# Kernel tuning notes

Measured on AMD Instinct MI355X. Metric: run time of the kernel, lower is better.

Reference implementation:

```python
import jax, jax.numpy as jnp
import numpy as np

# Dims: T timesteps, B batch, C channels, HID expert hidden, E experts, K top-k
T, B, C, HID, E, K, H, W = 4, 8, 256, 1024, 8, 2, 14, 14
EPS = 1e-5       # BatchNorm eps
ALPHA = 4.0      # spikingjelly sigmoid surrogate alpha
V_TH = 1.0       # LIF threshold (spikingjelly default), v_reset = 0.0


@jax.custom_vjp
def spike_fn(u):
    # Heaviside forward, sigmoid-surrogate backward (spikingjelly surrogate.Sigmoid)
    return (u >= 0.0).astype(u.dtype)

def _spike_fwd(u):
    return (u >= 0.0).astype(u.dtype), u

def _spike_bwd(u, g):
    s = jax.nn.sigmoid(ALPHA * u)
    return (g * ALPHA * s * (1.0 - s),)

spike_fn.defvjp(_spike_fwd, _spike_bwd)


def lif(x, tau):
    """MultiStepLIFNode with hard reset (v_reset=0), detach_reset=True.
    x: (T, B, C, H, W) -> spikes of same shape."""
    def step(v, xt):
        h = v + (xt - v) / tau                      # charge
        s = spike_fn(h - V_TH)                      # fire
        v_new = h * (1.0 - jax.lax.stop_gradient(s))  # hard reset, detached spike
        return v_new, s
    _, spikes = jax.lax.scan(step, jnp.zeros_like(x[0]), x)
    return spikes


def conv1x1(x, w, b):
    # x: (T,B,Cin,H,W), w: (Cout,Cin), b: (Cout,) -- 1x1 conv == channel GEMM
    return jnp.einsum('tbchw,oc->tbohw', x, w) + b[None, None, :, None, None]


def bn(x, g, b, m, v, axis):
    # inference-mode BatchNorm with running stats, per-channel on `axis`
    shp = [1] * x.ndim
    shp[axis] = -1
    scale = g.reshape(shp) / jnp.sqrt(v.reshape(shp) + EPS)
    return (x - m.reshape(shp)) * scale + b.reshape(shp)


def expert(x, tau, w1, b1, g1, be1, m1, v1, w2, b2, g2, be2, m2, v2):
    # MS_MLP_Expert.forward: lif -> conv1x1 -> bn -> lif -> conv1x1 -> bn (no residual)
    s1 = lif(x, tau)
    h = bn(conv1x1(s1, w1, b1), g1, be1, m1, v1, axis=2)  # (T,B,HID,H,W)
    s2 = lif(h, tau)
    return bn(conv1x1(s2, w2, b2), g2, be2, m2, v2, axis=2)  # (T,B,C,H,W)


def setup_inputs() -> dict:
    key = jax.random.key(0)
    ks = jax.random.split(key, 16)
    d = {}
    d['x'] = jax.random.normal(ks[0], (T, B, C, H, W), jnp.float32)
    # router (Conv2d(C, E, 1) + BatchNorm2d(E))
    d['router_w'] = jax.random.normal(ks[1], (E, C), jnp.float32) / np.sqrt(C)
    d['router_b'] = jax.random.normal(ks[2], (E,), jnp.float32) * 0.01
    d['rbn_g'] = 1.0 + 0.1 * jax.random.normal(ks[3], (E,), jnp.float32)
    d['rbn_b'] = 0.1 * jax.random.normal(ks[4], (E,), jnp.float32)
    d['rbn_m'] = 0.1 * jax.random.normal(ks[5], (E,), jnp.float32)
    d['rbn_v'] = jax.random.uniform(ks[6], (E,), jnp.float32, 0.5, 1.5)
    # stacked expert params (leading expert axis E)
    d['fc1_w'] = jax.random.normal(ks[7], (E, HID, C), jnp.float32) / np.sqrt(C)
    d['fc1_b'] = 0.01 * jax.random.normal(ks[8], (E, HID), jnp.float32)
    d['bn1_g'] = 1.0 + 0.1 * jax.random.normal(ks[9], (E, HID), jnp.float32)
    d['bn1_b'] = 0.1 * jax.random.normal(ks[10], (E, HID), jnp.float32)
    d['bn1_m'] = 0.1 * jax.random.normal(ks[11], (E, HID), jnp.float32)
    d['bn1_v'] = jax.random.uniform(ks[12], (E, HID), jnp.float32, 0.5, 1.5)
    d['fc2_w'] = jax.random.normal(ks[13], (E, C, HID), jnp.float32) / np.sqrt(HID)
    d['fc2_b'] = 0.01 * jax.random.normal(ks[14], (E, C), jnp.float32)
    d['bn2_g'] = 1.0 + 0.1 * jax.random.normal(ks[15], (E, C), jnp.float32)
    k2 = jax.random.split(jax.random.fold_in(key, 1), 3)
    d['bn2_b'] = 0.1 * jax.random.normal(k2[0], (E, C), jnp.float32)
    d['bn2_m'] = 0.1 * jax.random.normal(k2[1], (E, C), jnp.float32)
    d['bn2_v'] = jax.random.uniform(k2[2], (E, C), jnp.float32, 0.5, 1.5)
    # expert taus: linspace(tau_min=1.5, tau_max=4.0, num_experts)
    d['taus'] = jnp.linspace(1.5, 4.0, E, dtype=jnp.float32)
    return d


def reference(x, router_w, router_b, rbn_g, rbn_b, rbn_m, rbn_v,
              fc1_w, fc1_b, bn1_g, bn1_b, bn1_m, bn1_v,
              fc2_w, fc2_b, bn2_g, bn2_b, bn2_m, bn2_v, taus):
    b_sz = x.shape[1]
    # ---- TemporalRouter ----
    xm = x.mean(axis=0)                                           # (B,C,H,W)
    r = jnp.einsum('bchw,ec->behw', xm, router_w) + router_b[None, :, None, None]
    r = bn(r, rbn_g, rbn_b, rbn_m, rbn_v, axis=1)
    logits = r.mean(axis=(-2, -1))                                # (B,E)
    probs = jax.nn.softmax(logits, axis=-1)
    topw, topi = jax.lax.top_k(probs, K)                          # (B,K)
    topw = topw / topw.sum(axis=-1, keepdims=True)
    # dense combine weights (B,E): top-k entries, 0 elsewhere; detached as in torch
    Wd = jnp.zeros((b_sz, E), x.dtype).at[jnp.arange(b_sz)[:, None], topi].add(topw)
    Wd = jax.lax.stop_gradient(Wd)
    # ---- Experts (dense dispatch: each expert over full batch, masked combine) ----
    outs = jax.vmap(expert, in_axes=(None,) + (0,) * 13)(
        x, taus, fc1_w, fc1_b, bn1_g, bn1_b, bn1_m, bn1_v,
        fc2_w, fc2_b, bn2_g, bn2_b, bn2_m, bn2_v)                 # (E,T,B,C,H,W)
    moe = jnp.einsum('etbchw,be->tbchw', outs, Wd)
    return x + moe
```

## Files before the change

kernel.cpp:

```cpp
#include <hip/hip_runtime.h>
#include <hip/hip_bf16.h>
#include <math.h>

#define T_ 4
#define B_ 8
#define C_ 256
#define HID_ 1024
#define E_ 8
#define K_ 2
#define HW_ 196
#define M_ 784
#define NPAIR_ 16
#define EPS_ 1e-5f

typedef __attribute__((ext_vector_type(8))) short bf16x8;
typedef __attribute__((ext_vector_type(8))) unsigned short u16x8;
typedef __attribute__((ext_vector_type(4))) float f32x4;

__device__ inline unsigned short f2bf(float f){
  union { float f; unsigned u; } v; v.f = f;
  unsigned u = v.u;
  unsigned r = u + 0x7FFFu + ((u >> 16) & 1u);
  return (unsigned short)(r >> 16);
}
__device__ inline float bf2f(unsigned short h){
  union { unsigned u; float f; } v; v.u = ((unsigned)h) << 16;
  return v.f;
}

__global__ __launch_bounds__(256) void wconv_kernel(const float* __restrict__ w,
    unsigned short* __restrict__ hi, unsigned short* __restrict__ lo, int n){
  int i = blockIdx.x * 256 + threadIdx.x;
  if (i >= n) return;
  float f = w[i];
  unsigned short h = f2bf(f);
  hi[i] = h;
  lo[i] = f2bf(f - bf2f(h));
}

__global__ __launch_bounds__(64) void xbar_kernel(const float* __restrict__ x,
                                                  float* __restrict__ xbar){
  int bc = blockIdx.x;
  int l = threadIdx.x;
  float s = 0.f;
  for (int t = 0; t < T_; t++){
    const float* p = x + ((size_t)(t * B_ * C_) + bc) * HW_;
    for (int i = l; i < HW_; i += 64) s += p[i];
  }
  for (int off = 32; off > 0; off >>= 1) s += __shfl_down(s, off, 64);
  if (l == 0) xbar[bc] = s * (1.0f / (T_ * HW_));
}

__global__ __launch_bounds__(64) void router_kernel(const float* __restrict__ xbar,
    const float* __restrict__ rw, const float* __restrict__ rb,
    const float* __restrict__ rg, const float* __restrict__ rbb,
    const float* __restrict__ rm, const float* __restrict__ rv,
    int* __restrict__ sel_e, float* __restrict__ sel_w){
  __shared__ float lg[64];
  const int tid = threadIdx.x;
  const int b = tid >> 3, e = tid & 7;
  float dot = 0.f;
  for (int c = 0; c < C_; c++) dot += xbar[b * C_ + c] * rw[e * C_ + c];
  dot += rb[e];
  float sc = rg[e] / sqrtf(rv[e] + EPS_);
  lg[tid] = (dot - rm[e]) * sc + rbb[e];
  __syncthreads();
  if (e == 0){
    float l[E_], mx = -1e30f;
    for (int i = 0; i < E_; i++){ l[i] = lg[b * 8 + i]; mx = fmaxf(mx, l[i]); }
    float p[E_];
    for (int i = 0; i < E_; i++) p[i] = expf(l[i] - mx);
    int i1 = 0;
    for (int i = 1; i < E_; i++) if (p[i] > p[i1]) i1 = i;
    int i2 = (i1 == 0) ? 1 : 0;
    for (int i = 0; i < E_; i++) if (i != i1 && p[i] > p[i2]) i2 = i;
    float denom = p[i1] + p[i2];
    sel_e[b * 2]     = i1; sel_w[b * 2]     = p[i1] / denom;
    sel_e[b * 2 + 1] = i2; sel_w[b * 2 + 1] = p[i2] / denom;
  }
}

__global__ __launch_bounds__(256) void lif1_kernel(const float* __restrict__ x,
    const int* __restrict__ sel_e, const float* __restrict__ taus,
    unsigned short* __restrict__ s1){
  const int hw = blockIdx.x;
  const int pair = blockIdx.y;
  const int c = threadIdx.x;
  const int b = pair >> 1;
  const float tau = taus[sel_e[pair]];
  float v = 0.f;
  #pragma unroll
  for (int t = 0; t < T_; t++){
    float xv = x[((size_t)(t * B_ + b) * C_ + c) * HW_ + hw];
    float h = v + (xv - v) / tau;
    float s = (h >= 1.0f) ? 1.0f : 0.0f;
    v = h * (1.0f - s);
    s1[((size_t)pair * M_ + hw * 4 + t) * C_ + c] =
        (s > 0.5f) ? (unsigned short)0x3F80 : (unsigned short)0;
  }
}

__global__ __launch_bounds__(256) void g1_kernel(
    const unsigned short* __restrict__ s1,
    const unsigned short* __restrict__ w1h, const unsigned short* __restrict__ w1l,
    const float* __restrict__ fc1_b,
    const float* __restrict__ bn1_g, const float* __restrict__ bn1_b,
    const float* __restrict__ bn1_m, const float* __restrict__ bn1_v,
    const int* __restrict__ sel_e, const float* __restrict__ taus,
    unsigned short* __restrict__ s2)
{
  __shared__ __align__(16) unsigned short lA[64 * 40];
  __shared__ __align__(16) unsigned short lBh[64 * 40];
  __shared__ __align__(16) unsigned short lBl[64 * 40];
  const int nt = blockIdx.x, mt = blockIdx.y, pair = blockIdx.z;
  const int e = sel_e[pair];
  const int m0 = mt * 64, n0 = nt * 64;
  const int tid = threadIdx.x;
  const int row = tid >> 2, seg = tid & 3;
  const int lane = tid & 63, wv = tid >> 6;
  const int koff = (lane >> 4) * 8;
  const unsigned short* s1p = s1 + (size_t)pair * (M_ * C_);
  const unsigned short* bhp = w1h + ((size_t)e * HID_ + n0 + row) * C_ + seg * 8;
  const unsigned short* blp = w1l + ((size_t)e * HID_ + n0 + row) * C_ + seg * 8;
  f32x4 acc[4] = {};
  for (int kk = 0; kk < C_; kk += 32){
    int r = m0 + row;
    u16x8 av = {};
    if (r < M_) av = *(const u16x8*)(s1p + (size_t)r * C_ + kk + seg * 8);
    *(u16x8*)(lA  + row * 40 + seg * 8) = av;
    *(u16x8*)(lBh + row * 40 + seg * 8) = *(const u16x8*)(bhp + kk);
    *(u16x8*)(lBl + row * 40 + seg * 8) = *(const u16x8*)(blp + kk);
    __syncthreads();
    bf16x8 a = *(const bf16x8*)(lA + (wv * 16 + (lane & 15)) * 40 + koff);
    #pragma unroll
    for (int cb = 0; cb < 4; cb++){
      bf16x8 bh = *(const bf16x8*)(lBh + (cb * 16 + (lane & 15)) * 40 + koff);
      bf16x8 bl = *(const bf16x8*)(lBl + (cb * 16 + (lane & 15)) * 40 + koff);
      acc[cb] = __builtin_amdgcn_mfma_f32_16x16x32_bf16(a, bh, acc[cb], 0, 0, 0);
      acc[cb] = __builtin_amdgcn_mfma_f32_16x16x32_bf16(a, bl, acc[cb], 0, 0, 0);
    }
    __syncthreads();
  }
  const float tau = taus[e];
  const int rbase = m0 + wv * 16 + ((lane >> 4) << 2);
  if (rbase < M_){
    #pragma unroll
    for (int cb = 0; cb < 4; cb++){
      int col = n0 + cb * 16 + (lane & 15);
      int pi = e * HID_ + col;
      float sc = bn1_g[pi] / sqrtf(bn1_v[pi] + EPS_);
      float mm = bn1_m[pi], bb = bn1_b[pi], cbias = fc1_b[pi];
      float v = 0.f;
      #pragma unroll
      for (int t = 0; t < 4; t++){
        float z = acc[cb][t] + cbias;
        float hin = (z - mm) * sc + bb;
        float h = v + (hin - v) / tau;
        float s = (h >= 1.0f) ? 1.0f : 0.0f;
        v = h * (1.0f - s);
        s2[((size_t)pair * M_ + rbase + t) * HID_ + col] =
            (s > 0.5f) ? (unsigned short)0x3F80 : (unsigned short)0;
      }
    }
  }
}

__global__ __launch_bounds__(256) void g2_kernel(
    const unsigned short* __restrict__ s2,
    const unsigned short* __restrict__ w2h, const unsigned short* __restrict__ w2l,
    const float* __restrict__ fc2_b,
    const float* __restrict__ bn2_g, const float* __restrict__ bn2_b,
    const float* __restrict__ bn2_m, const float* __restrict__ bn2_v,
    const int* __restrict__ sel_e, const float* __restrict__ sel_w,
    const float* __restrict__ x, float* __restrict__ out)
{
  __shared__ __align__(16) unsigned short lA[64 * 40];
  __shared__ __align__(16) unsigned short lBh[64 * 40];
  __shared__ __align__(16) unsigned short lBl[64 * 40];
  const int nt = blockIdx.x, mt = blockIdx.y, b = blockIdx.z;
  const int m0 = mt * 64, n0 = nt * 64;
  const int tid = threadIdx.x;
  const int row = tid >> 2, seg = tid & 3;
  const int lane = tid & 63, wv = tid >> 6;
  const int koff = (lane >> 4) * 8;
  f32x4 res[4] = {};
  for (int slot = 0; slot < 2; slot++){
    const int pair = b * 2 + slot;
    const int e = sel_e[pair];
    const float wgt = sel_w[pair];
    const unsigned short* s2p = s2 + (size_t)pair * (M_ * HID_);
    const unsigned short* bhp = w2h + ((size_t)e * C_ + n0 + row) * HID_ + seg * 8;
    const unsigned short* blp = w2l + ((size_t)e * C_ + n0 + row) * HID_ + seg * 8;
    f32x4 acc[4] = {};
    for (int kk = 0; kk < HID_; kk += 32){
      int r = m0 + row;
      u16x8 av = {};
      if (r < M_) av = *(const u16x8*)(s2p + (size_t)r * HID_ + kk + seg * 8);
      *(u16x8*)(lA  + row * 40 + seg * 8) = av;
      *(u16x8*)(lBh + row * 40 + seg * 8) = *(const u16x8*)(bhp + kk);
      *(u16x8*)(lBl + row * 40 + seg * 8) = *(const u16x8*)(blp + kk);
      __syncthreads();
      bf16x8 a = *(const bf16x8*)(lA + (wv * 16 + (lane & 15)) * 40 + koff);
      #pragma unroll
      for (int cb = 0; cb < 4; cb++){
        bf16x8 bh = *(const bf16x8*)(lBh + (cb * 16 + (lane & 15)) * 40 + koff);
        bf16x8 bl = *(const bf16x8*)(lBl + (cb * 16 + (lane & 15)) * 40 + koff);
        acc[cb] = __builtin_amdgcn_mfma_f32_16x16x32_bf16(a, bh, acc[cb], 0, 0, 0);
        acc[cb] = __builtin_amdgcn_mfma_f32_16x16x32_bf16(a, bl, acc[cb], 0, 0, 0);
      }
      __syncthreads();
    }
    #pragma unroll
    for (int cb = 0; cb < 4; cb++){
      int col = n0 + cb * 16 + (lane & 15);
      int pi = e * C_ + col;
      float sc = bn2_g[pi] / sqrtf(bn2_v[pi] + EPS_);
      float mm = bn2_m[pi], bb = bn2_b[pi], cbias = fc2_b[pi];
      #pragma unroll
      for (int t = 0; t < 4; t++){
        float z = acc[cb][t] + cbias;
        float y = (z - mm) * sc + bb;
        res[cb][t] += wgt * y;
      }
    }
  }
  const int rbase = m0 + wv * 16 + ((lane >> 4) << 2);
  if (rbase < M_){
    const int hw = rbase >> 2;
    #pragma unroll
    for (int cb = 0; cb < 4; cb++){
      int col = n0 + cb * 16 + (lane & 15);
      #pragma unroll
      for (int t = 0; t < 4; t++){
        size_t oi = ((size_t)(t * B_ + b) * C_ + col) * HW_ + hw;
        out[oi] = x[oi] + res[cb][t];
      }
    }
  }
}

extern "C" void kernel_launch(void* const* d_in, const int* in_sizes, int n_in,
                              void* d_out, int out_size, void* d_ws, size_t ws_size,
                              hipStream_t stream){
  const float* x     = (const float*)d_in[0];
  const float* rw    = (const float*)d_in[1];
  const float* rb    = (const float*)d_in[2];
  const float* rg    = (const float*)d_in[3];
  const float* rbb   = (const float*)d_in[4];
  const float* rm    = (const float*)d_in[5];
  const float* rv    = (const float*)d_in[6];
  const float* fc1_w = (const float*)d_in[7];
  const float* fc1_b = (const float*)d_in[8];
  const float* bn1_g = (const float*)d_in[9];
  const float* bn1_b = (const float*)d_in[10];
  const float* bn1_m = (const float*)d_in[11];
  const float* bn1_v = (const float*)d_in[12];
  const float* fc2_w = (const float*)d_in[13];
  const float* fc2_b = (const float*)d_in[14];
  const float* bn2_g = (const float*)d_in[15];
  const float* bn2_b = (const float*)d_in[16];
  const float* bn2_m = (const float*)d_in[17];
  const float* bn2_v = (const float*)d_in[18];
  const float* taus  = (const float*)d_in[19];
  float* out = (float*)d_out;

  char* ws = (char*)d_ws;
  size_t off = 0;
  auto alloc = [&](size_t bytes) -> char* {
    char* p = ws + off;
    off = (off + bytes + 255) & ~(size_t)255;
    return p;
  };
  const int NW = E_ * HID_ * C_;
  unsigned short* w1h = (unsigned short*)alloc((size_t)NW * 2);
  unsigned short* w1l = (unsigned short*)alloc((size_t)NW * 2);
  unsigned short* w2h = (unsigned short*)alloc((size_t)NW * 2);
  unsigned short* w2l = (unsigned short*)alloc((size_t)NW * 2);
  unsigned short* s1  = (unsigned short*)alloc((size_t)NPAIR_ * M_ * C_ * 2);
  unsigned short* s2  = (unsigned short*)alloc((size_t)NPAIR_ * M_ * HID_ * 2);
  float* xbar  = (float*)alloc(B_ * C_ * 4);
  int*   sel_e = (int*)alloc(NPAIR_ * 4);
  float* sel_w = (float*)alloc(NPAIR_ * 4);
  (void)ws_size; (void)in_sizes; (void)n_in; (void)out_size;

  wconv_kernel<<<(NW + 255) / 256, 256, 0, stream>>>(fc1_w, w1h, w1l, NW);
  wconv_kernel<<<(NW + 255) / 256, 256, 0, stream>>>(fc2_w, w2h, w2l, NW);
  xbar_kernel<<<B_ * C_, 64, 0, stream>>>(x, xbar);
  router_kernel<<<1, 64, 0, stream>>>(xbar, rw, rb, rg, rbb, rm, rv, sel_e, sel_w);
  lif1_kernel<<<dim3(HW_, NPAIR_), 256, 0, stream>>>(x, sel_e, taus, s1);
  g1_kernel<<<dim3(HID_ / 64, (M_ + 63) / 64, NPAIR_), 256, 0, stream>>>(
      s1, w1h, w1l, fc1_b, bn1_g, bn1_b, bn1_m, bn1_v, sel_e, taus, s2);
  g2_kernel<<<dim3(C_ / 64, (M_ + 63) / 64, B_), 256, 0, stream>>>(
      s2, w2h, w2l, fc2_b, bn2_g, bn2_b, bn2_m, bn2_v, sel_e, sel_w, x, out);
}
```

Before: 226.8 us.

## Fuse weight bf16 split into GEMMs, double-buffer LDS, drop low-part in second GEMM

Removes the two standalone weight-conversion kernels and converts fp32 weights to bf16 hi/lo on the fly inside the GEMM load path. g1 now keeps the whole spike A tile resident in LDS and loops over 512 output columns per block, with a double-buffered, register-prefetched B tile. g2 is double-buffered and uses only the bf16 high part of the weights, halving its MFMA count. The g2 change is exact only up to bf16 rounding of w2. g1 now has far fewer blocks, which reduces parallelism.

Result: no change. 230.8 us (+1.8%).

```diff
diff --git a/kernel.cpp b/kernel.cpp
--- a/kernel.cpp
+++ b/kernel.cpp
@@ -28,14 +28,23 @@
   return v.f;
 }
 
-__global__ __launch_bounds__(256) void wconv_kernel(const float* __restrict__ w,
-    unsigned short* __restrict__ hi, unsigned short* __restrict__ lo, int n){
-  int i = blockIdx.x * 256 + threadIdx.x;
-  if (i >= n) return;
-  float f = w[i];
-  unsigned short h = f2bf(f);
-  hi[i] = h;
-  lo[i] = f2bf(f - bf2f(h));
+__device__ inline void split8(float4 v0, float4 v1, u16x8& hv, u16x8& lv){
+  float f0=v0.x,f1=v0.y,f2=v0.z,f3=v0.w,f4=v1.x,f5=v1.y,f6=v1.z,f7=v1.w;
+  unsigned short h;
+  h=f2bf(f0); hv[0]=h; lv[0]=f2bf(f0-bf2f(h));
+  h=f2bf(f1); hv[1]=h; lv[1]=f2bf(f1-bf2f(h));
+  h=f2bf(f2); hv[2]=h; lv[2]=f2bf(f2-bf2f(h));
+  h=f2bf(f3); hv[3]=h; lv[3]=f2bf(f3-bf2f(h));
+  h=f2bf(f4); hv[4]=h; lv[4]=f2bf(f4-bf2f(h));
+  h=f2bf(f5); hv[5]=h; lv[5]=f2bf(f5-bf2f(h));
+  h=f2bf(f6); hv[6]=h; lv[6]=f2bf(f6-bf2f(h));
+  h=f2bf(f7); hv[7]=h; lv[7]=f2bf(f7-bf2f(h));
+}
+__device__ inline u16x8 hi8(float4 v0, float4 v1){
+  u16x8 hv;
+  hv[0]=f2bf(v0.x); hv[1]=f2bf(v0.y); hv[2]=f2bf(v0.z); hv[3]=f2bf(v0.w);
+  hv[4]=f2bf(v1.x); hv[5]=f2bf(v1.y); hv[6]=f2bf(v1.z); hv[7]=f2bf(v1.w);
+  return hv;
 }
 
 __global__ __launch_bounds__(64) void xbar_kernel(const float* __restrict__ x,
@@ -102,113 +111,153 @@
 
 __global__ __launch_bounds__(256) void g1_kernel(
     const unsigned short* __restrict__ s1,
-    const unsigned short* __restrict__ w1h, const unsigned short* __restrict__ w1l,
+    const float* __restrict__ w1,
     const float* __restrict__ fc1_b,
     const float* __restrict__ bn1_g, const float* __restrict__ bn1_b,
     const float* __restrict__ bn1_m, const float* __restrict__ bn1_v,
     const int* __restrict__ sel_e, const float* __restrict__ taus,
     unsigned short* __restrict__ s2)
 {
-  __shared__ __align__(16) unsigned short lA[64 * 40];
-  __shared__ __align__(16) unsigned short lBh[64 * 40];
-  __shared__ __align__(16) unsigned short lBl[64 * 40];
-  const int nt = blockIdx.x, mt = blockIdx.y, pair = blockIdx.z;
+  __shared__ __align__(16) unsigned short lA[8][64 * 40];
+  __shared__ __align__(16) unsigned short lBh[2][64 * 40];
+  __shared__ __align__(16) unsigned short lBl[2][64 * 40];
+  const int nhalf = blockIdx.x, mt = blockIdx.y, pair = blockIdx.z;
   const int e = sel_e[pair];
-  const int m0 = mt * 64, n0 = nt * 64;
+  const int m0 = mt * 64;
   const int tid = threadIdx.x;
   const int row = tid >> 2, seg = tid & 3;
   const int lane = tid & 63, wv = tid >> 6;
   const int koff = (lane >> 4) * 8;
-  const unsigned short* s1p = s1 + (size_t)pair * (M_ * C_);
-  const unsigned short* bhp = w1h + ((size_t)e * HID_ + n0 + row) * C_ + seg * 8;
-  const unsigned short* blp = w1l + ((size_t)e * HID_ + n0 + row) * C_ + seg * 8;
-  f32x4 acc[4] = {};
-  for (int kk = 0; kk < C_; kk += 32){
-    int r = m0 + row;
-    u16x8 av = {};
-    if (r < M_) av = *(const u16x8*)(s1p + (size_t)r * C_ + kk + seg * 8);
-    *(u16x8*)(lA  + row * 40 + seg * 8) = av;
-    *(u16x8*)(lBh + row * 40 + seg * 8) = *(const u16x8*)(bhp + kk);
-    *(u16x8*)(lBl + row * 40 + seg * 8) = *(const u16x8*)(blp + kk);
-    __syncthreads();
-    bf16x8 a = *(const bf16x8*)(lA + (wv * 16 + (lane & 15)) * 40 + koff);
+  {
+    const unsigned short* s1p = s1 + (size_t)pair * (M_ * C_);
+    const int r = m0 + row;
     #pragma unroll
-    for (int cb = 0; cb < 4; cb++){
-      bf16x8 bh = *(const bf16x8*)(lBh + (cb * 16 + (lane & 15)) * 40 + koff);
-      bf16x8 bl = *(const bf16x8*)(lBl + (cb * 16 + (lane & 15)) * 40 + koff);
-      acc[cb] = __builtin_amdgcn_mfma_f32_16x16x32_bf16(a, bh, acc[cb], 0, 0, 0);
-      acc[cb] = __builtin_amdgcn_mfma_f32_16x16x32_bf16(a, bl, acc[cb], 0, 0, 0);
-    }
-    __syncthreads();
-  }
+    for (int ch = 0; ch < 8; ch++){
+      u16x8 av = {};
+      if (r < M_) av = *(const u16x8*)(s1p + (size_t)r * C_ + ch * 32 + seg * 8);
+      *(u16x8*)(&lA[ch][row * 40 + seg * 8]) = av;
+    }
+  }
+  const float* wp = w1 + ((size_t)e * HID_ + nhalf * 512 + row) * C_ + seg * 8;
+  {
+    const float4* p = (const float4*)wp;
+    float4 v0 = p[0], v1 = p[1];
+    u16x8 hv, lv; split8(v0, v1, hv, lv);
+    *(u16x8*)(&lBh[0][row * 40 + seg * 8]) = hv;
+    *(u16x8*)(&lBl[0][row * 40 + seg * 8]) = lv;
+  }
+  __syncthreads();
   const float tau = taus[e];
   const int rbase = m0 + wv * 16 + ((lane >> 4) << 2);
-  if (rbase < M_){
-    #pragma unroll
-    for (int cb = 0; cb < 4; cb++){
-      int col = n0 + cb * 16 + (lane & 15);
-      int pi = e * HID_ + col;
-      float sc = bn1_g[pi] / sqrtf(bn1_v[pi] + EPS_);
-      float mm = bn1_m[pi], bb = bn1_b[pi], cbias = fc1_b[pi];
-      float v = 0.f;
+  int cur = 0;
+  for (int nt = 0; nt < 8; nt++){
+    f32x4 acc[4] = {};
+    for (int kk = 0; kk < 8; kk++){
+      const int ii = nt * 8 + kk;
+      const bool nx = (ii < 63);
+      float4 v0, v1;
+      if (nx){
+        const int jj = ii + 1;
+        const float4* p = (const float4*)(wp + (size_t)(jj >> 3) * 64 * C_ + (jj & 7) * 32);
+        v0 = p[0]; v1 = p[1];
+      }
+      bf16x8 a = *(const bf16x8*)(&lA[kk][(wv * 16 + (lane & 15)) * 40 + koff]);
       #pragma unroll
-      for (int t = 0; t < 4; t++){
-        float z = acc[cb][t] + cbias;
-        float hin = (z - mm) * sc + bb;
-        float h = v + (hin - v) / tau;
-        float s = (h >= 1.0f) ? 1.0f : 0.0f;
-        v = h * (1.0f - s);
-        s2[((size_t)pair * M_ + rbase + t) * HID_ + col] =
-            (s > 0.5f) ? (unsigned short)0x3F80 : (unsigned short)0;
-      }
+      for (int cb = 0; cb < 4; cb++){
+        bf16x8 bh = *(const bf16x8*)(&lBh[cur][(cb * 16 + (lane & 15)) * 40 + koff]);
+        bf16x8 bl = *(const bf16x8*)(&lBl[cur][(cb * 16 + (lane & 15)) * 40 + koff]);
+        acc[cb] = __builtin_amdgcn_mfma_f32_16x16x32_bf16(a, bh, acc[cb], 0, 0, 0);
+        acc[cb] = __builtin_amdgcn_mfma_f32_16x16x32_bf16(a, bl, acc[cb], 0, 0, 0);
+      }
+      if (nx){
+        u16x8 hv, lv; split8(v0, v1, hv, lv);
+        *(u16x8*)(&lBh[cur ^ 1][row * 40 + seg * 8]) = hv;
+        *(u16x8*)(&lBl[cur ^ 1][row * 40 + seg * 8]) = lv;
+      }
+      if (kk == 7 && rbase < M_){
+        #pragma unroll
+        for (int cb = 0; cb < 4; cb++){
+          int col = nhalf * 512 + nt * 64 + cb * 16 + (lane & 15);
+          int pi = e * HID_ + col;
+          float sc = bn1_g[pi] / sqrtf(bn1_v[pi] + EPS_);
+          float mm = bn1_m[pi], bb = bn1_b[pi], cbias = fc1_b[pi];
+          float v = 0.f;
+          #pragma unroll
+          for (int t = 0; t < 4; t++){
+            float z = acc[cb][t] + cbias;
+            float hin = (z - mm) * sc + bb;
+            float h = v + (hin - v) / tau;
+            float s = (h >= 1.0f) ? 1.0f : 0.0f;
+            v = h * (1.0f - s);
+            s2[((size_t)pair * M_ + rbase + t) * HID_ + col] =
+                (s > 0.5f) ? (unsigned short)0x3F80 : (unsigned short)0;
+          }
+        }
+      }
+      __syncthreads();
+      cur ^= 1;
     }
   }
 }
 
 __global__ __launch_bounds__(256) void g2_kernel(
     const unsigned short* __restrict__ s2,
-    const unsigned short* __restrict__ w2h, const unsigned short* __restrict__ w2l,
+    const float* __restrict__ w2,
     const float* __restrict__ fc2_b,
     const float* __restrict__ bn2_g, const float* __restrict__ bn2_b,
     const float* __restrict__ bn2_m, const float* __restrict__ bn2_v,
     const int* __restrict__ sel_e, const float* __restrict__ sel_w,
     const float* __restrict__ x, float* __restrict__ out)
 {
-  __shared__ __align__(16) unsigned short lA[64 * 40];
-  __shared__ __align__(16) unsigned short lBh[64 * 40];
-  __shared__ __align__(16) unsigned short lBl[64 * 40];
+  __shared__ __align__(16) unsigned short lA[2][64 * 40];
+  __shared__ __align__(16) unsigned short lBh[2][64 * 40];
   const int nt = blockIdx.x, mt = blockIdx.y, b = blockIdx.z;
   const int m0 = mt * 64, n0 = nt * 64;
   const int tid = threadIdx.x;
   const int row = tid >> 2, seg = tid & 3;
   const int lane = tid & 63, wv = tid >> 6;
   const int koff = (lane >> 4) * 8;
+  const int r = m0 + row;
   f32x4 res[4] = {};
   for (int slot = 0; slot < 2; slot++){
     const int pair = b * 2 + slot;
     const int e = sel_e[pair];
     const float wgt = sel_w[pair];
-    const unsigned short* s2p = s2 + (size_t)pair * (M_ * HID_);
-    const unsigned short* bhp = w2h + ((size_t)e * C_ + n0 + row) * HID_ + seg * 8;
-    const unsigned short* blp = w2l + ((size_t)e * C_ + n0 + row) * HID_ + seg * 8;
+    const unsigned short* s2p = s2 + (size_t)pair * (M_ * HID_) + (size_t)r * HID_ + seg * 8;
+    const float* wp = w2 + ((size_t)e * C_ + n0 + row) * HID_ + seg * 8;
+    {
+      u16x8 av = {};
+      if (r < M_) av = *(const u16x8*)s2p;
+      const float4* p = (const float4*)wp;
+      u16x8 hv = hi8(p[0], p[1]);
+      *(u16x8*)(&lA[0][row * 40 + seg * 8]) = av;
+      *(u16x8*)(&lBh[0][row * 40 + seg * 8]) = hv;
+    }
+    __syncthreads();
     f32x4 acc[4] = {};
-    for (int kk = 0; kk < HID_; kk += 32){
-      int r = m0 + row;
+    int cur = 0;
+    for (int kk = 0; kk < 32; kk++){
+      const bool nx = (kk < 31);
       u16x8 av = {};
-      if (r < M_) av = *(const u16x8*)(s2p + (size_t)r * HID_ + kk + seg * 8);
-      *(u16x8*)(lA  + row * 40 + seg * 8) = av;
-      *(u16x8*)(lBh + row * 40 + seg * 8) = *(const u16x8*)(bhp + kk);
-      *(u16x8*)(lBl + row * 40 + seg * 8) = *(const u16x8*)(blp + kk);
-      __syncthreads();
-      bf16x8 a = *(const bf16x8*)(lA + (wv * 16 + (lane & 15)) * 40 + koff);
+      float4 v0, v1;
+      if (nx){
+        if (r < M_) av = *(const u16x8*)(s2p + (kk + 1) * 32);
+        const float4* p = (const float4*)(wp + (kk + 1) * 32);
+        v0 = p[0]; v1 = p[1];
+      }
+      bf16x8 a = *(const bf16x8*)(&lA[cur][(wv * 16 + (lane & 15)) * 40 + koff]);
       #pragma unroll
       for (int cb = 0; cb < 4; cb++){
-        bf16x8 bh = *(const bf16x8*)(lBh + (cb * 16 + (lane & 15)) * 40 + koff);
-        bf16x8 bl = *(const bf16x8*)(lBl + (cb * 16 + (lane & 15)) * 40 + koff);
+        bf16x8 bh = *(const bf16x8*)(&lBh[cur][(cb * 16 + (lane & 15)) * 40 + koff]);
         acc[cb] = __builtin_amdgcn_mfma_f32_16x16x32_bf16(a, bh, acc[cb], 0, 0, 0);
-        acc[cb] = __builtin_amdgcn_mfma_f32_16x16x32_bf16(a, bl, acc[cb], 0, 0, 0);
+      }
+      if (nx){
+        u16x8 hv = hi8(v0, v1);
+        *(u16x8*)(&lA[cur ^ 1][row * 40 + seg * 8]) = av;
+        *(u16x8*)(&lBh[cur ^ 1][row * 40 + seg * 8]) = hv;
       }
       __syncthreads();
+      cur ^= 1;
     }
     #pragma unroll
     for (int cb = 0; cb < 4; cb++){
@@ -271,11 +320,6 @@
     off = (off + bytes + 255) & ~(size_t)255;
     return p;
   };
-  const int NW = E_ * HID_ * C_;
-  unsigned short* w1h = (unsigned short*)alloc((size_t)NW * 2);
-  unsigned short* w1l = (unsigned short*)alloc((size_t)NW * 2);
-  unsigned short* w2h = (unsigned short*)alloc((size_t)NW * 2);
-  unsigned short* w2l = (unsigned short*)alloc((size_t)NW * 2);
   unsigned short* s1  = (unsigned short*)alloc((size_t)NPAIR_ * M_ * C_ * 2);
   unsigned short* s2  = (unsigned short*)alloc((size_t)NPAIR_ * M_ * HID_ * 2);
   float* xbar  = (float*)alloc(B_ * C_ * 4);
@@ -283,13 +327,11 @@
   float* sel_w = (float*)alloc(NPAIR_ * 4);
   (void)ws_size; (void)in_sizes; (void)n_in; (void)out_size;
 
-  wconv_kernel<<<(NW + 255) / 256, 256, 0, stream>>>(fc1_w, w1h, w1l, NW);
-  wconv_kernel<<<(NW + 255) / 256, 256, 0, stream>>>(fc2_w, w2h, w2l, NW);
   xbar_kernel<<<B_ * C_, 64, 0, stream>>>(x, xbar);
   router_kernel<<<1, 64, 0, stream>>>(xbar, rw, rb, rg, rbb, rm, rv, sel_e, sel_w);
   lif1_kernel<<<dim3(HW_, NPAIR_), 256, 0, stream>>>(x, sel_e, taus, s1);
-  g1_kernel<<<dim3(HID_ / 64, (M_ + 63) / 64, NPAIR_), 256, 0, stream>>>(
-      s1, w1h, w1l, fc1_b, bn1_g, bn1_b, bn1_m, bn1_v, sel_e, taus, s2);
+  g1_kernel<<<dim3(2, (M_ + 63) / 64, NPAIR_), 256, 0, stream>>>(
+      s1, fc1_w, fc1_b, bn1_g, bn1_b, bn1_m, bn1_v, sel_e, taus, s2);
   g2_kernel<<<dim3(C_ / 64, (M_ + 63) / 64, B_), 256, 0, stream>>>(
-      s2, w2h, w2l, fc2_b, bn2_g, bn2_b, bn2_m, bn2_v, sel_e, sel_w, x, out);
-}
+      s2, fc2_w, fc2_b, bn2_g, bn2_b, bn2_m, bn2_v, sel_e, sel_w, x, out);
+}
```
